# Kernel tuning notes

Measured on AMD Instinct MI355X. Metric: run time of the kernel, lower is better.

Reference implementation:

```python
import jax, jax.numpy as jnp
import numpy as np

DELTA = 0.1625
FREQ_SCALE = 0.325
MIN_LAYERS = 1
MAX_LAYERS = 5
EPS = 1e-12  # F.normalize eps


def _l2norm(x, axis):
    n = jnp.sqrt(jnp.sum(x * x, axis=axis, keepdims=True))
    return x / jnp.maximum(n, EPS)


def setup_inputs() -> dict:
    key = jax.random.key(0)
    k1, k2, k3 = jax.random.split(key, 3)
    B, N, D = 8, 2048, 64
    embeddings = jax.random.normal(k1, (B, N, D), dtype=jnp.float32)
    # scale to [0, 15) so echo_layers spans the full 1..5 range
    frequencies = jax.random.uniform(k2, (B, N), dtype=jnp.float32) * 15.0
    relationship_matrix = jax.random.uniform(k3, (B, N, N), dtype=jnp.float32)
    return {"embeddings": embeddings, "frequencies": frequencies,
            "relationship_matrix": relationship_matrix}


def reference(embeddings, frequencies, relationship_matrix):
    B, N, D = embeddings.shape
    # per-token number of echo iterations
    echo_layers = jnp.clip(
        MIN_LAYERS + jnp.floor(frequencies * FREQ_SCALE), MIN_LAYERS, MAX_LAYERS
    ).astype(jnp.int32)  # [B, N]

    refined = _l2norm(embeddings, axis=2)  # [B, N, D]

    # mask out the diagonal of the relationship matrix once (it is constant
    # across layers); shifts[i] = delta * sum_j rm[i,j]*(e_i - e_j)
    #               = delta * (e_i * rowsum[i] - (rm @ e)[i])
    rm = relationship_matrix * (1.0 - jnp.eye(N, dtype=relationship_matrix.dtype))
    rowsum = jnp.sum(rm, axis=-1)  # [B, N]

    def step(e, layer):
        active = (layer < echo_layers)[..., None].astype(e.dtype)  # [B, N, 1]
        agg = jnp.einsum('bij,bjd->bid', rm, e)                     # [B, N, D]
        shifts = DELTA * (e * rowsum[..., None] - agg)
        upd = _l2norm(e + shifts * active, axis=2)
        # tokens with zero shift are already unit-norm, so renorm is identity
        return upd, None

    refined, _ = jax.lax.scan(step, refined, jnp.arange(MAX_LAYERS))
    return refined
```

## Files before the change

### kernel.cpp

```cpp
#include <hip/hip_runtime.h>
#include <stdint.h>

#define BB 8
#define NN 2048
#define DD 64
#define DELTA 0.1625f
#define FREQ_SCALE 0.325f

typedef __bf16 bf16x8 __attribute__((ext_vector_type(8)));
typedef float f32x4 __attribute__((ext_vector_type(4)));
typedef unsigned int u32x4 __attribute__((ext_vector_type(4)));
typedef unsigned int u32x2 __attribute__((ext_vector_type(2)));

static __device__ __forceinline__ unsigned short f2b(float x) {
    union { float f; unsigned int u; } c; c.f = x;
    unsigned int r = (c.u + 0x7FFFu + ((c.u >> 16) & 1u)) >> 16;
    return (unsigned short)r;
}

static __device__ __forceinline__ void gl_lds16(const void* g, void* l) {
    __builtin_amdgcn_global_load_lds(
        (const __attribute__((address_space(1))) void*)g,
        (__attribute__((address_space(3))) void*)l, 16, 0, 0);
}

__global__ __launch_bounds__(256) void prep_norm(
        const float* __restrict__ emb, const float* __restrict__ freq,
        float* __restrict__ e0, unsigned short* __restrict__ eT0,
        int* __restrict__ echo) {
    __shared__ unsigned short tile[64][72];
    int t = threadIdx.x;
    int tok0 = blockIdx.x * 64;
    int lt = t >> 2;
    int tt = tok0 + lt;
    int dd = (t & 3) * 16;

    const float* src = emb + (size_t)tt * DD + dd;
    f32x4 v[4];
    float ss = 0.f;
    #pragma unroll
    for (int q = 0; q < 4; q++) {
        v[q] = *(const f32x4*)(src + q * 4);
        ss += v[q].x*v[q].x + v[q].y*v[q].y + v[q].z*v[q].z + v[q].w*v[q].w;
    }
    ss += __shfl_xor(ss, 1);
    ss += __shfl_xor(ss, 2);
    float scale = 1.f / fmaxf(sqrtf(ss), 1e-12f);
    float* dst = e0 + (size_t)tt * DD + dd;
    #pragma unroll
    for (int q = 0; q < 4; q++) {
        f32x4 o = v[q] * scale;
        *(f32x4*)(dst + q * 4) = o;
        tile[lt][dd + q*4 + 0] = f2b(o.x);
        tile[lt][dd + q*4 + 1] = f2b(o.y);
        tile[lt][dd + q*4 + 2] = f2b(o.z);
        tile[lt][dd + q*4 + 3] = f2b(o.w);
    }
    if ((t & 3) == 0) {
        int el = 1 + (int)floorf(freq[tt] * FREQ_SCALE);
        el = el < 1 ? 1 : (el > 5 ? 5 : el);
        echo[tt] = el;
    }
    __syncthreads();
    int b  = tok0 / NN;
    int tb = tok0 % NN;
    for (int idx = t; idx < 64 * 64; idx += 256) {
        int d = idx >> 6, j = idx & 63;
        eT0[((size_t)b * DD + d) * NN + tb + j] = tile[j][d];
    }
}

template<bool WRB>
__global__ __launch_bounds__(256) void cast_rowsum(
        const float* __restrict__ rm, unsigned short* __restrict__ rmb,
        float* __restrict__ rowsum) {
    int gw = (int)((blockIdx.x * 256 + threadIdx.x) >> 6);
    int l = threadIdx.x & 63;
    const float* src = rm + (size_t)gw * NN;
    f32x4 v[8];
    #pragma unroll
    for (int q = 0; q < 8; q++)
        v[q] = *(const f32x4*)(src + q * 256 + l * 4);
    float s = 0.f;
    #pragma unroll
    for (int q = 0; q < 8; q++)
        s += (v[q].x + v[q].y) + (v[q].z + v[q].w);
    if constexpr (WRB) {
        unsigned short* dst = rmb + (size_t)gw * NN;
        #pragma unroll
        for (int q = 0; q < 8; q++) {
            u32x2 o;
            o.x = (unsigned)f2b(v[q].x) | ((unsigned)f2b(v[q].y) << 16);
            o.y = (unsigned)f2b(v[q].z) | ((unsigned)f2b(v[q].w) << 16);
            *(u32x2*)(dst + q * 256 + l * 4) = o;
        }
    }
    #pragma unroll
    for (int m = 1; m < 64; m <<= 1) s += __shfl_xor(s, m);
    if (l == 0) rowsum[gw] = s;
}

__global__ __launch_bounds__(512, 1) void layer_fused(
        const unsigned short* __restrict__ rmb,
        const unsigned short* __restrict__ eT_src,
        const float* __restrict__ e_src,
        const float* __restrict__ rowsum_g,
        const int* __restrict__ echo,
        float* __restrict__ e_dst,
        unsigned short* __restrict__ eT_dst,
        int layer) {
    __shared__ char SB4[4][8192];
    __shared__ char SA4[4][8192];
    __shared__ float redSS[4][2][16];

    const int t = threadIdx.x;
    const int w = t >> 6, l = t & 63;
    const int lo = l & 15, hi = l >> 4;
    const int it = w & 3, dh = w >> 2;
    const int i0 = blockIdx.x * 64;
    const int b  = blockIdx.y;

    const char* rmB = (const char*)(rmb + ((size_t)b * NN + i0) * NN);
    const char* eTB = (const char*)(eT_src + (size_t)b * DD * NN);

    const size_t srow = (size_t)(w * 8 + (l >> 3)) * (NN * 2);
    const int csrc = ((l & 7) ^ (l >> 3)) << 4;

    f32x4 acc0 = {}, acc1 = {};

    const int rowB  = it * 16 + lo;
    const int rowA0 = dh * 32 + lo;
    const int rowA1 = dh * 32 + 16 + lo;
    const int xr = (lo & 7) << 4;

#define ISSUE(bi, step) do {                                       \
    const int ksb = (step) * 128;                                  \
    gl_lds16(rmB + srow + ksb + csrc, &SB4[bi][w * 1024]);         \
    gl_lds16(eTB + srow + ksb + csrc, &SA4[bi][w * 1024]);         \
} while (0)

#define COMP(bi) do {                                              \
    _Pragma("unroll")                                              \
    for (int kk = 0; kk < 2; kk++) {                               \
        int co = ((kk << 6) | (hi << 4)) ^ xr;                     \
        u32x4 fB  = *(const u32x4*)(&SB4[bi][rowB  * 128 + co]);   \
        u32x4 fA0 = *(const u32x4*)(&SA4[bi][rowA0 * 128 + co]);   \
        u32x4 fA1 = *(const u32x4*)(&SA4[bi][rowA1 * 128 + co]);   \
        acc0 = __builtin_amdgcn_mfma_f32_16x16x32_bf16(            \
            __builtin_bit_cast(bf16x8, fA0), __builtin_bit_cast(bf16x8, fB), acc0, 0, 0, 0); \
        acc1 = __builtin_amdgcn_mfma_f32_16x16x32_bf16(            \
            __builtin_bit_cast(bf16x8, fA1), __builtin_bit_cast(bf16x8, fB), acc1, 0, 0, 0); \
    }                                                              \
} while (0)

    ISSUE(0, 0);
    ISSUE(1, 1);
    ISSUE(2, 2);
    #pragma unroll
    for (int s = 0; s < 32; s++) {
        if (s < 30)      asm volatile("s_waitcnt vmcnt(4)" ::: "memory");
        else if (s == 30) asm volatile("s_waitcnt vmcnt(2)" ::: "memory");
        else             asm volatile("s_waitcnt vmcnt(0)" ::: "memory");
        __builtin_amdgcn_s_barrier();
        __builtin_amdgcn_sched_barrier(0);
        if (s < 29) {
            const int nb = (s + 3) & 3;
            if (nb == 0)      ISSUE(0, s + 3);
            else if (nb == 1) ISSUE(1, s + 3);
            else if (nb == 2) ISSUE(2, s + 3);
            else              ISSUE(3, s + 3);
        }
        const int cb = s & 3;
        if (cb == 0)      COMP(0);
        else if (cb == 1) COMP(1);
        else if (cb == 2) COMP(2);
        else              COMP(3);
    }
#undef ISSUE
#undef COMP

    const size_t gi = (size_t)b * NN + i0 + it * 16 + lo;
    const float rs = rowsum_g[gi];
    const float coef = (layer < echo[gi]) ? DELTA : 0.f;
    const size_t eb = gi * DD + dh * 32 + hi * 4;
    f32x4 e0 = *(const f32x4*)(e_src + eb);
    f32x4 e1 = *(const f32x4*)(e_src + eb + 16);
    f32x4 u0 = e0 + coef * (e0 * rs - acc0);
    f32x4 u1 = e1 + coef * (e1 * rs - acc1);
    float ss = u0.x*u0.x + u0.y*u0.y + u0.z*u0.z + u0.w*u0.w
             + u1.x*u1.x + u1.y*u1.y + u1.z*u1.z + u1.w*u1.w;
    ss += __shfl_xor(ss, 16);
    ss += __shfl_xor(ss, 32);
    if (hi == 0) redSS[it][dh][lo] = ss;
    __syncthreads();
    float sst = redSS[it][0][lo] + redSS[it][1][lo];
    float scale = 1.f / fmaxf(sqrtf(sst), 1e-12f);
    u0 *= scale;
    u1 *= scale;
    *(f32x4*)(e_dst + eb) = u0;
    *(f32x4*)(e_dst + eb + 16) = u1;
    unsigned short* ep = eT_dst + (size_t)b * DD * NN;
    const int i = i0 + it * 16 + lo;
    const int d0 = dh * 32 + hi * 4;
    ep[(size_t)(d0 + 0)  * NN + i] = f2b(u0.x);
    ep[(size_t)(d0 + 1)  * NN + i] = f2b(u0.y);
    ep[(size_t)(d0 + 2)  * NN + i] = f2b(u0.z);
    ep[(size_t)(d0 + 3)  * NN + i] = f2b(u0.w);
    ep[(size_t)(d0 + 16) * NN + i] = f2b(u1.x);
    ep[(size_t)(d0 + 17) * NN + i] = f2b(u1.y);
    ep[(size_t)(d0 + 18) * NN + i] = f2b(u1.z);
    ep[(size_t)(d0 + 19) * NN + i] = f2b(u1.w);
}

__global__ __launch_bounds__(512, 4) void layer_step_fb(
        const float* __restrict__ rm_,
        const unsigned short* __restrict__ eT_src,
        const float* __restrict__ e_src,
        const float* __restrict__ rowsum_g,
        const int* __restrict__ echo,
        float* __restrict__ e_dst,
        unsigned short* __restrict__ eT_dst,
        int layer) {
    __shared__ float redAcc[3][2][64][20];

    int t = threadIdx.x;
    int w = t >> 6, l = t & 63;
    int b = blockIdx.y;
    int i0 = blockIdx.x * 32;
    int wi = w & 1;
    int kq = w >> 1;
    int lane_lo = l & 15, lane_hi = l >> 4;
    int i = i0 + wi * 16 + lane_lo;
    size_t gi = (size_t)b * NN + i;
    int kbase = kq * (NN / 4) + 8 * lane_hi;

    int echo_pre = echo[gi];
    float rs = rowsum_g[gi];

    const unsigned short* eT_b = eT_src + (size_t)b * DD * NN;
    const unsigned short* ea0 = eT_b + (size_t)(lane_lo)      * NN + kbase;
    const unsigned short* ea1 = eT_b + (size_t)(16 + lane_lo) * NN + kbase;
    const unsigned short* ea2 = eT_b + (size_t)(32 + lane_lo) * NN + kbase;
    const unsigned short* ea3 = eT_b + (size_t)(48 + lane_lo) * NN + kbase;

    f32x4 acc[4] = {};
    const float* rmp32 = rm_ + gi * NN + kbase;

    #pragma unroll
    for (int j = 0; j < 16; j++) {
        const int o = 32 * j;
        f32x4 lo4 = *(const f32x4*)(rmp32 + o);
        f32x4 hi4 = *(const f32x4*)(rmp32 + o + 4);
        u32x4 ob;
        ob.x = (unsigned)f2b(lo4.x) | ((unsigned)f2b(lo4.y) << 16);
        ob.y = (unsigned)f2b(lo4.z) | ((unsigned)f2b(lo4.w) << 16);
        ob.z = (unsigned)f2b(hi4.x) | ((unsigned)f2b(hi4.y) << 16);
        ob.w = (unsigned)f2b(hi4.z) | ((unsigned)f2b(hi4.w) << 16);
        bf16x8 bfrag = __builtin_bit_cast(bf16x8, ob);
        acc[0] = __builtin_amdgcn_mfma_f32_16x16x32_bf16(
            __builtin_bit_cast(bf16x8, *(const u32x4*)(ea0 + o)), bfrag, acc[0], 0, 0, 0);
        acc[1] = __builtin_amdgcn_mfma_f32_16x16x32_bf16(
            __builtin_bit_cast(bf16x8, *(const u32x4*)(ea1 + o)), bfrag, acc[1], 0, 0, 0);
        acc[2] = __builtin_amdgcn_mfma_f32_16x16x32_bf16(
            __builtin_bit_cast(bf16x8, *(const u32x4*)(ea2 + o)), bfrag, acc[2], 0, 0, 0);
        acc[3] = __builtin_amdgcn_mfma_f32_16x16x32_bf16(
            __builtin_bit_cast(bf16x8, *(const u32x4*)(ea3 + o)), bfrag, acc[3], 0, 0, 0);
    }

    if (kq > 0) {
        #pragma unroll
        for (int f = 0; f < 4; f++)
            *(f32x4*)(&redAcc[kq - 1][wi][l][4 * f]) = acc[f];
    }
    __syncthreads();
    if (kq == 0) {
        #pragma unroll
        for (int f = 0; f < 4; f++) {
            acc[f] += *(const f32x4*)(&redAcc[0][wi][l][4 * f]);
            acc[f] += *(const f32x4*)(&redAcc[1][wi][l][4 * f]);
            acc[f] += *(const f32x4*)(&redAcc[2][wi][l][4 * f]);
        }
        float coef = DELTA * ((layer < echo_pre) ? 1.f : 0.f);
        size_t ebase = gi * DD;
        f32x4 upd[4];
        float ss = 0.f;
        #pragma unroll
        for (int f = 0; f < 4; f++) {
            f32x4 e = *(const f32x4*)(e_src + ebase + 16 * f + 4 * lane_hi);
            f32x4 u = e + coef * (e * rs - acc[f]);
            upd[f] = u;
            ss += u.x*u.x + u.y*u.y + u.z*u.z + u.w*u.w;
        }
        ss += __shfl_xor(ss, 16);
        ss += __shfl_xor(ss, 32);
        float scale = 1.f / fmaxf(sqrtf(ss), 1e-12f);
        unsigned short* ep = eT_dst + (size_t)b * DD * NN;
        #pragma unroll
        for (int f = 0; f < 4; f++) {
            f32x4 o = upd[f] * scale;
            *(f32x4*)(e_dst + ebase + 16 * f + 4 * lane_hi) = o;
            int dbase = 16 * f + 4 * lane_hi;
            ep[(size_t)(dbase + 0) * NN + i] = f2b(o.x);
            ep[(size_t)(dbase + 1) * NN + i] = f2b(o.y);
            ep[(size_t)(dbase + 2) * NN + i] = f2b(o.z);
            ep[(size_t)(dbase + 3) * NN + i] = f2b(o.w);
        }
    }
}

extern "C" void kernel_launch(void* const* d_in, const int* in_sizes, int n_in,
                              void* d_out, int out_size, void* d_ws, size_t ws_size,
                              hipStream_t stream) {
    const float* emb  = (const float*)d_in[0];
    const float* freq = (const float*)d_in[1];
    const float* rm   = (const float*)d_in[2];
    float* out = (float*)d_out;
    char* ws = (char*)d_ws;

    const size_t eBytes   = (size_t)BB * NN * DD * 4;
    const size_t eTBytes  = (size_t)BB * DD * NN * 2;
    const size_t bnBytes  = (size_t)BB * NN * 4;
    const size_t rmbBytes = (size_t)BB * NN * NN * 2;
    float* e_f32[2] = { (float*)ws, (float*)(ws + eBytes) };
    unsigned short* eT[2] = { (unsigned short*)(ws + 2*eBytes),
                              (unsigned short*)(ws + 2*eBytes + eTBytes) };
    float* rowsum = (float*)(ws + 2*eBytes + 2*eTBytes);
    int* echo = (int*)(ws + 2*eBytes + 2*eTBytes + bnBytes);
    unsigned short* rmb = (unsigned short*)(ws + 2*eBytes + 2*eTBytes + 2*bnBytes);
    size_t need_cached = 2*eBytes + 2*eTBytes + 2*bnBytes + rmbBytes;

    int cached = (ws_size >= need_cached) ? 1 : 0;

    prep_norm<<<dim3(BB*NN/64), dim3(256), 0, stream>>>(emb, freq, e_f32[0], eT[0], echo);

    if (cached) {
        cast_rowsum<true><<<dim3(BB*NN/4), dim3(256), 0, stream>>>(rm, rmb, rowsum);
        for (int l = 0; l < 5; l++) {
            float* dst = (l == 4) ? out : e_f32[(l + 1) & 1];
            layer_fused<<<dim3(NN/64, BB), dim3(512), 0, stream>>>(
                rmb, eT[l & 1], e_f32[l & 1], rowsum, echo,
                dst, eT[(l + 1) & 1], l);
        }
    } else {
        cast_rowsum<false><<<dim3(BB*NN/4), dim3(256), 0, stream>>>(rm, nullptr, rowsum);
        for (int l = 0; l < 5; l++) {
            float* dst = (l == 4) ? out : e_f32[(l + 1) & 1];
            layer_step_fb<<<dim3(NN/32, BB), dim3(512), 0, stream>>>(
                rm, eT[l & 1], e_f32[l & 1], rowsum, echo,
                dst, eT[(l + 1) & 1], l);
        }
    }
}
```

Before: 126.3 us.

## Deepen LDS prefetch pipeline to six stages, raise MFMA priority, interleave batch blocks

The layer kernel's global-to-LDS prefetch ring grows from 4 to 6 buffers, with 5 stages in flight and the vmcnt waits adjusted to match, so more memory latency is hidden behind the MFMA work. The compute section raises wave priority with s_setprio while its MFMAs run. The grid is flattened to 1D with the batch index in the low bits, so neighbouring blocks come from different batches. LDS use grows to about 96KB per block, which is fine with one block per CU but limits occupancy headroom.

```diff
diff --git a/kernel.cpp b/kernel.cpp
--- a/kernel.cpp
+++ b/kernel.cpp
@@ -109,16 +109,17 @@
         float* __restrict__ e_dst,
         unsigned short* __restrict__ eT_dst,
         int layer) {
-    __shared__ char SB4[4][8192];
-    __shared__ char SA4[4][8192];
+    __shared__ char SB6[6][8192];
+    __shared__ char SA6[6][8192];
     __shared__ float redSS[4][2][16];
 
     const int t = threadIdx.x;
     const int w = t >> 6, l = t & 63;
     const int lo = l & 15, hi = l >> 4;
     const int it = w & 3, dh = w >> 2;
-    const int i0 = blockIdx.x * 64;
-    const int b  = blockIdx.y;
+    const int gid = blockIdx.x;
+    const int b  = gid & 7;
+    const int i0 = (gid >> 3) * 64;
 
     const char* rmB = (const char*)(rmb + ((size_t)b * NN + i0) * NN);
     const char* eTB = (const char*)(eT_src + (size_t)b * DD * NN);
@@ -135,46 +136,55 @@
 
 #define ISSUE(bi, step) do {                                       \
     const int ksb = (step) * 128;                                  \
-    gl_lds16(rmB + srow + ksb + csrc, &SB4[bi][w * 1024]);         \
-    gl_lds16(eTB + srow + ksb + csrc, &SA4[bi][w * 1024]);         \
+    gl_lds16(rmB + srow + ksb + csrc, &SB6[bi][w * 1024]);         \
+    gl_lds16(eTB + srow + ksb + csrc, &SA6[bi][w * 1024]);         \
 } while (0)
 
 #define COMP(bi) do {                                              \
+    __builtin_amdgcn_s_setprio(1);                                 \
     _Pragma("unroll")                                              \
     for (int kk = 0; kk < 2; kk++) {                               \
         int co = ((kk << 6) | (hi << 4)) ^ xr;                     \
-        u32x4 fB  = *(const u32x4*)(&SB4[bi][rowB  * 128 + co]);   \
-        u32x4 fA0 = *(const u32x4*)(&SA4[bi][rowA0 * 128 + co]);   \
-        u32x4 fA1 = *(const u32x4*)(&SA4[bi][rowA1 * 128 + co]);   \
+        u32x4 fB  = *(const u32x4*)(&SB6[bi][rowB  * 128 + co]);   \
+        u32x4 fA0 = *(const u32x4*)(&SA6[bi][rowA0 * 128 + co]);   \
+        u32x4 fA1 = *(const u32x4*)(&SA6[bi][rowA1 * 128 + co]);   \
         acc0 = __builtin_amdgcn_mfma_f32_16x16x32_bf16(            \
             __builtin_bit_cast(bf16x8, fA0), __builtin_bit_cast(bf16x8, fB), acc0, 0, 0, 0); \
         acc1 = __builtin_amdgcn_mfma_f32_16x16x32_bf16(            \
             __builtin_bit_cast(bf16x8, fA1), __builtin_bit_cast(bf16x8, fB), acc1, 0, 0, 0); \
     }                                                              \
+    __builtin_amdgcn_s_setprio(0);                                 \
 } while (0)
 
     ISSUE(0, 0);
     ISSUE(1, 1);
     ISSUE(2, 2);
+    ISSUE(3, 3);
+    ISSUE(4, 4);
     #pragma unroll
     for (int s = 0; s < 32; s++) {
-        if (s < 30)      asm volatile("s_waitcnt vmcnt(4)" ::: "memory");
+        if (s < 29)       asm volatile("s_waitcnt vmcnt(8)" ::: "memory");
+        else if (s == 29) asm volatile("s_waitcnt vmcnt(4)" ::: "memory");
         else if (s == 30) asm volatile("s_waitcnt vmcnt(2)" ::: "memory");
-        else             asm volatile("s_waitcnt vmcnt(0)" ::: "memory");
+        else              asm volatile("s_waitcnt vmcnt(0)" ::: "memory");
         __builtin_amdgcn_s_barrier();
         __builtin_amdgcn_sched_barrier(0);
-        if (s < 29) {
-            const int nb = (s + 3) & 3;
-            if (nb == 0)      ISSUE(0, s + 3);
-            else if (nb == 1) ISSUE(1, s + 3);
-            else if (nb == 2) ISSUE(2, s + 3);
-            else              ISSUE(3, s + 3);
-        }
-        const int cb = s & 3;
+        if (s < 27) {
+            const int nb = (s + 5) % 6;
+            if (nb == 0)      ISSUE(0, s + 5);
+            else if (nb == 1) ISSUE(1, s + 5);
+            else if (nb == 2) ISSUE(2, s + 5);
+            else if (nb == 3) ISSUE(3, s + 5);
+            else if (nb == 4) ISSUE(4, s + 5);
+            else              ISSUE(5, s + 5);
+        }
+        const int cb = s % 6;
         if (cb == 0)      COMP(0);
         else if (cb == 1) COMP(1);
         else if (cb == 2) COMP(2);
-        else              COMP(3);
+        else if (cb == 3) COMP(3);
+        else if (cb == 4) COMP(4);
+        else              COMP(5);
     }
 #undef ISSUE
 #undef COMP
@@ -337,7 +347,7 @@
         cast_rowsum<true><<<dim3(BB*NN/4), dim3(256), 0, stream>>>(rm, rmb, rowsum);
         for (int l = 0; l < 5; l++) {
             float* dst = (l == 4) ? out : e_f32[(l + 1) & 1];
-            layer_fused<<<dim3(NN/64, BB), dim3(512), 0, stream>>>(
+            layer_fused<<<dim3(256), dim3(512), 0, stream>>>(
                 rmb, eT[l & 1], e_f32[l & 1], rowsum, echo,
                 dst, eT[(l + 1) & 1], l);
         }
```

Result: faster. 119.3 us (-5.5%).
